# Kernel tuning notes

Hardware: AMD Instinct MI355X
Metric: run time of the kernel (lower is better)

The kernel has to match this reference:

```python
import jax, jax.numpy as jnp
import numpy as np

DT = 1.0 / 120.0
B, T = 2048, 2048


def setup_inputs() -> dict:
    key = jax.random.key(0)
    k1, k2 = jax.random.split(key)
    # friction, damping, restitution (restitution only affects the collision
    # branch, which is not exercised by the non-colliding reference dynamics)
    params = jax.random.uniform(k1, (3,), jnp.float32, 0.05, 0.9)
    # smooth synthetic trajectories: cumulative small steps of [x, y, theta]
    meas = jnp.cumsum(jax.random.normal(k2, (B, T, 3), jnp.float32) * 0.01, axis=1)
    return {"params": params, "measurements": meas}


def _ekf_loss(params, measurements):
    friction, damping = params[0], params[1]
    dt = jnp.asarray(DT, measurements.dtype)
    dtype = measurements.dtype

    R = jnp.diag(jnp.array([2.5e-7, 2.5e-7, 9.1e-3], dtype=dtype))
    Q = jnp.diag(jnp.array([2e-10, 2e-10, 3e-7, 3e-7, 1e-2, 1e-1], dtype=dtype))
    H = jnp.zeros((3, 6), dtype=dtype).at[0, 0].set(1.0).at[1, 1].set(1.0).at[2, 4].set(1.0)
    I6 = jnp.eye(6, dtype=dtype)

    # linearized transition Jacobian (constant-velocity with table damping)
    F = I6
    F = F.at[0, 2].set(dt).at[1, 3].set(dt).at[4, 5].set(dt)
    F = F.at[2, 2].set(1.0 - dt * damping).at[3, 3].set(1.0 - dt * damping)

    def predict_state(s):
        x, y, dx, dy, th, dth = s
        dx2 = dx - dt * (damping * dx + friction * jnp.sign(dx))
        dy2 = dy - dt * (damping * dy + friction * jnp.sign(dy))
        return jnp.stack([x + dx * dt, y + dy * dt, dx2, dy2, th + dth * dt, dth])

    def step(carry, z):
        s, P, acc = carry
        s_pred = predict_state(s)                     # (6,)
        P_pred = F @ P @ F.T + Q                      # (6,6)
        yv = z - H @ s_pred                           # (3,) innovation
        S = H @ P_pred @ H.T + R                      # (3,3)
        Sinv_y = jnp.linalg.solve(S, yv)
        K = jnp.linalg.solve(S.T, (P_pred @ H.T).T).T  # P_pred H^T S^{-1}
        s_new = s_pred + K @ yv
        P_new = (I6 - K @ H) @ P_pred
        # evaluation term: sign*exp(logdet(S)) + y^T S^{-1} y == det(S) + y^T S^{-1} y
        acc = acc + jnp.linalg.det(S) + yv @ Sinv_y
        return (s_new, P_new, acc), None

    def run_one(zs):
        # initial state from finite-difference velocities (as in the source)
        v0 = (zs[1] - zs[0]) / dt
        s0 = jnp.stack([zs[0, 0], zs[0, 1], v0[0], v0[1], zs[0, 2], v0[2]])
        P0 = I6 * 0.01
        (_, _, acc), _ = jax.lax.scan(step, (s0, P0, jnp.zeros((), dtype)), zs[1:])
        return acc / (zs.shape[0] - 1)

    return jnp.mean(jax.vmap(run_one)(measurements))


def reference(params, measurements):
    return _ekf_loss(params, measurements)
```

## Files before the change

kernel.cpp:

```cpp
#include <hip/hip_runtime.h>

#define DTF (1.0f/120.0f)

constexpr int Bn = 2048;
constexpr int Tn = 2048;
constexpr int NS = Tn - 1;
constexpr int ZF = Tn * 3;
constexpr int NCH = 64;
constexpr int LCH = 32;
constexpr int SPAN = 109;
constexpr int NSEG = 14;
constexpr int BT = 64;
constexpr int GX = Bn / BT;
constexpr int NBLK = GX * NCH;
constexpr int LSTR = 66;

__global__ __launch_bounds__(BT, 2) void ekf_main(const float* __restrict__ params,
                                                  const float* __restrict__ meas,
                                                  double* __restrict__ part)
{
    __shared__ float lds[28 * LSTR];

    const int tid = threadIdx.x;
    const int c = blockIdx.y;
    const float dt = DTF;
    const float fric = params[0];
    const float damping = params[1];
    const float a = 1.f - dt * damping;
    const float dfr = dt * fric;
    const float dt2 = dt * dt, a2 = a * a;
    const float qp = 2e-10f, qv = 3e-7f, qth = 1e-2f, qdth = 1e-1f;
    const float Rp = 2.5e-7f, Rt = 9.1e-3f;
    const float* __restrict__ zt = meas + (size_t)(blockIdx.x * BT) * ZF;

    const int j0   = c * LCH;
    const int jend = min(j0 + LCH, NS);
    int jw = jend - SPAN;
    jw = (jw < 3) ? 0 : (jw - ((jw - 3) & 3));
    const int A0 = (jw * 3 + 3) & ~3;
    const int d  = jw * 3 + 3 - A0;
    const int AI = (jw * 3) & ~3;
    const int di = jw * 3 - AI;

    float4 g[7];
#define LOADF(A) do { \
    _Pragma("unroll") \
    for (int i_ = 0; i_ < 7; ++i_) { \
        int flat_ = i_ * BT + tid; \
        int row_ = flat_ / 7, k_ = flat_ - row_ * 7; \
        int fs_ = min((A) + 4 * k_, ZF - 4); \
        g[i_] = *(const float4*)(zt + (size_t)row_ * ZF + fs_); \
    } \
} while (0)
#define STORELDS() do { \
    _Pragma("unroll") \
    for (int i_ = 0; i_ < 7; ++i_) { \
        int flat_ = i_ * BT + tid; \
        int row_ = flat_ / 7, k_ = flat_ - row_ * 7; \
        int base_ = 4 * k_ * LSTR + row_; \
        lds[base_]            = g[i_].x; \
        lds[base_ + LSTR]     = g[i_].y; \
        lds[base_ + 2*LSTR]   = g[i_].z; \
        lds[base_ + 3*LSTR]   = g[i_].w; \
    } \
} while (0)

    LOADF(AI);
    STORELDS();
    float i0 = lds[(di+0)*LSTR + tid], i1 = lds[(di+1)*LSTR + tid], i2 = lds[(di+2)*LSTR + tid];
    float i3 = lds[(di+3)*LSTR + tid], i4 = lds[(di+4)*LSTR + tid], i5 = lds[(di+5)*LSTR + tid];
    float s0 = i0, s1 = i1, s4 = i2;
    float s2 = (i3 - i0) / dt, s3 = (i4 - i1) / dt, s5 = (i5 - i2) / dt;

    float x00 = 0.01f, x01 = 0.f, x11 = 0.01f;
    float t00 = 0.01f, t01 = 0.f, t11 = 0.01f;

    LOADF(A0);
    float facc = 0.f;

    for (int s = 0; s < NSEG; ++s) {
        STORELDS();
        LOADF(A0 + 24 * (s + 1));
        __builtin_amdgcn_sched_barrier(0);
        float zv[24];
        #pragma unroll
        for (int k2 = 0; k2 < 24; ++k2) zv[k2] = lds[(d + k2) * LSTR + tid];
        const int jb = jw + 8 * s;
        #pragma unroll
        for (int ss = 0; ss < 8; ++ss) {
            float Pp00 = fmaf(dt2, x11, fmaf(2.f * dt, x01, x00)) + qp;
            float Pp01 = a * fmaf(dt, x11, x01);
            float Pp11 = fmaf(a2, x11, qv);
            float Sx = Pp00 + Rp;
            float isx = __builtin_amdgcn_rcpf(Sx);
            float kx0 = Pp00 * isx, kx1 = Pp01 * isx;
            x00 = Pp00 - kx0 * Pp00; x01 = Pp01 - kx0 * Pp01; x11 = Pp11 - kx1 * Pp01;
            float Tp00 = fmaf(dt2, t11, fmaf(2.f * dt, t01, t00)) + qth;
            float Tp01 = fmaf(dt, t11, t01);
            float Tp11 = t11 + qdth;
            float St = Tp00 + Rt;
            float ist = __builtin_amdgcn_rcpf(St);
            float kt0 = Tp00 * ist, kt1 = Tp01 * ist;
            t00 = Tp00 - kt0 * Tp00; t01 = Tp01 - kt0 * Tp01; t11 = Tp11 - kt1 * Tp01;
            float det = Sx * Sx * St;
            float p0 = fmaf(dt, s2, s0), p1 = fmaf(dt, s3, s1), p4 = fmaf(dt, s5, s4);
            float p2 = fmaf(a, s2, -copysignf(dfr, s2));
            float p3 = fmaf(a, s3, -copysignf(dfr, s3));
            float y0 = zv[ss*3+0] - p0, y1 = zv[ss*3+1] - p1, y2 = zv[ss*3+2] - p4;
            s0 = fmaf(kx0, y0, p0); s1 = fmaf(kx0, y1, p1);
            s2 = fmaf(kx1, y0, p2); s3 = fmaf(kx1, y1, p3);
            s4 = fmaf(kt0, y2, p4); s5 = fmaf(kt1, y2, s5);
            int j = jb + ss;
            if (j >= j0 && j < jend)
                facc += det + isx * fmaf(y0, y0, y1 * y1) + ist * y2 * y2;
        }
    }
#undef STORELDS
#undef LOADF

    double acc = (double)facc;
    for (int off = 32; off; off >>= 1) acc += __shfl_down(acc, off);
    if (tid == 0) part[blockIdx.y * GX + blockIdx.x] = acc;
}

__global__ void finalize_kernel(const double* __restrict__ part, float* __restrict__ out)
{
    const int tid = threadIdx.x;
    double v = part[tid] + part[tid + 1024];
    for (int off = 32; off; off >>= 1) v += __shfl_down(v, off);
    __shared__ double wp[16];
    if ((tid & 63) == 0) wp[tid >> 6] = v;
    __syncthreads();
    if (tid == 0) {
        double t = 0.0;
        #pragma unroll
        for (int i = 0; i < 16; ++i) t += wp[i];
        out[0] = (float)(t / ((double)Bn * (double)NS));
    }
}

extern "C" void kernel_launch(void* const* d_in, const int* in_sizes, int n_in,
                              void* d_out, int out_size, void* d_ws, size_t ws_size,
                              hipStream_t stream)
{
    const float* params = (const float*)d_in[0];
    const float* meas = (const float*)d_in[1];
    double* part = (double*)d_ws;
    float* out = (float*)d_out;

    hipLaunchKernelGGL(ekf_main, dim3(GX, NCH), dim3(BT), 0, stream, params, meas, part);
    hipLaunchKernelGGL(finalize_kernel, dim3(1), dim3(1024), 0, stream, part, out);
}
```

Before: 39.34 us.

## Precompute shared Kalman gain table once and halve chunk length with more chunks

The covariance and gain recursion does not depend on the measurements, so it is now run once by a single-thread kernel that writes a per-step table of gains, inverse innovations and determinants. The main kernel loads this table into LDS and only does the state update, and chunks shrink to 16 steps over a shorter warm-up span with 128 chunks, plus early exit from segments past the chunk end. This removes the redundant per-thread covariance math and shortens the serial dependency chain per block. In exchange it adds a serial kernel launch on the critical path and relies on the covariance converging within the shorter span, since every chunk reuses the same early-step gains for its warm-up window.

```diff
diff --git a/kernel.cpp b/kernel.cpp
--- a/kernel.cpp
+++ b/kernel.cpp
@@ -6,20 +6,58 @@
 constexpr int Tn = 2048;
 constexpr int NS = Tn - 1;
 constexpr int ZF = Tn * 3;
-constexpr int NCH = 64;
-constexpr int LCH = 32;
-constexpr int SPAN = 109;
-constexpr int NSEG = 14;
+constexpr int NCH = 128;
+constexpr int LCH = 16;
+constexpr int SPAN = 88;
+constexpr int NSEG = 12;
+constexpr int GROWS = NSEG * 8;
 constexpr int BT = 64;
 constexpr int GX = Bn / BT;
 constexpr int NBLK = GX * NCH;
 constexpr int LSTR = 66;
+constexpr int GT_F = GROWS * 8;
 
-__global__ __launch_bounds__(BT, 2) void ekf_main(const float* __restrict__ params,
+constexpr int WS_PART = 4096;
+
+__global__ void gains_kernel(const float* __restrict__ params, float* __restrict__ gt)
+{
+    if (threadIdx.x != 0) return;
+    const float dt = DTF;
+    const float damping = params[1];
+    const float a = 1.f - dt * damping;
+    const float dt2 = dt * dt, a2 = a * a;
+    const float qp = 2e-10f, qv = 3e-7f, qth = 1e-2f, qdth = 1e-1f;
+    const float Rp = 2.5e-7f, Rt = 9.1e-3f;
+    float x00 = 0.01f, x01 = 0.f, x11 = 0.01f;
+    float t00 = 0.01f, t01 = 0.f, t11 = 0.01f;
+    for (int t = 0; t < GROWS; ++t) {
+        float Pp00 = fmaf(dt2, x11, fmaf(2.f * dt, x01, x00)) + qp;
+        float Pp01 = a * fmaf(dt, x11, x01);
+        float Pp11 = fmaf(a2, x11, qv);
+        float Sx = Pp00 + Rp;
+        float isx = __builtin_amdgcn_rcpf(Sx);
+        float kx0 = Pp00 * isx, kx1 = Pp01 * isx;
+        x00 = Pp00 - kx0 * Pp00; x01 = Pp01 - kx0 * Pp01; x11 = Pp11 - kx1 * Pp01;
+        float Tp00 = fmaf(dt2, t11, fmaf(2.f * dt, t01, t00)) + qth;
+        float Tp01 = fmaf(dt, t11, t01);
+        float Tp11 = t11 + qdth;
+        float St = Tp00 + Rt;
+        float ist = __builtin_amdgcn_rcpf(St);
+        float kt0 = Tp00 * ist, kt1 = Tp01 * ist;
+        t00 = Tp00 - kt0 * Tp00; t01 = Tp01 - kt0 * Tp01; t11 = Tp11 - kt1 * Tp01;
+        float* row = gt + (size_t)t * 8;
+        row[0] = kx0; row[1] = kx1; row[2] = kt0; row[3] = kt1;
+        row[4] = isx; row[5] = ist; row[6] = Sx * Sx * St; row[7] = 0.f;
+    }
+}
+
+__global__ __launch_bounds__(BT, 4) void ekf_main(const float* __restrict__ params,
                                                   const float* __restrict__ meas,
+                                                  const float* __restrict__ gt,
                                                   double* __restrict__ part)
 {
     __shared__ float lds[28 * LSTR];
+    __shared__ float gtab[GT_F];
 
     const int tid = threadIdx.x;
     const int c = blockIdx.y;
@@ -28,9 +66,6 @@
     const float damping = params[1];
     const float a = 1.f - dt * damping;
     const float dfr = dt * fric;
-    const float dt2 = dt * dt, a2 = a * a;
-    const float qp = 2e-10f, qv = 3e-7f, qth = 1e-2f, qdth = 1e-1f;
-    const float Rp = 2.5e-7f, Rt = 9.1e-3f;
     const float* __restrict__ zt = meas + (size_t)(blockIdx.x * BT) * ZF;
 
     const int j0   = c * LCH;
@@ -41,6 +76,9 @@
     const int d  = jw * 3 + 3 - A0;
     const int AI = (jw * 3) & ~3;
     const int di = jw * 3 - AI;
+
+    #pragma unroll
+    for (int i = 0; i < GT_F / BT; ++i) gtab[i * BT + tid] = gt[i * BT + tid];
 
     float4 g[7];
 #define LOADF(A) do { \
@@ -72,47 +110,32 @@
     float s0 = i0, s1 = i1, s4 = i2;
     float s2 = (i3 - i0) / dt, s3 = (i4 - i1) / dt, s5 = (i5 - i2) / dt;
 
-    float x00 = 0.01f, x01 = 0.f, x11 = 0.01f;
-    float t00 = 0.01f, t01 = 0.f, t11 = 0.01f;
-
     LOADF(A0);
     float facc = 0.f;
 
     for (int s = 0; s < NSEG; ++s) {
+        const int jb = jw + 8 * s;
+        if (jb >= jend) break;
         STORELDS();
         LOADF(A0 + 24 * (s + 1));
         __builtin_amdgcn_sched_barrier(0);
         float zv[24];
         #pragma unroll
         for (int k2 = 0; k2 < 24; ++k2) zv[k2] = lds[(d + k2) * LSTR + tid];
-        const int jb = jw + 8 * s;
         #pragma unroll
         for (int ss = 0; ss < 8; ++ss) {
-            float Pp00 = fmaf(dt2, x11, fmaf(2.f * dt, x01, x00)) + qp;
-            float Pp01 = a * fmaf(dt, x11, x01);
-            float Pp11 = fmaf(a2, x11, qv);
-            float Sx = Pp00 + Rp;
-            float isx = __builtin_amdgcn_rcpf(Sx);
-            float kx0 = Pp00 * isx, kx1 = Pp01 * isx;
-            x00 = Pp00 - kx0 * Pp00; x01 = Pp01 - kx0 * Pp01; x11 = Pp11 - kx1 * Pp01;
-            float Tp00 = fmaf(dt2, t11, fmaf(2.f * dt, t01, t00)) + qth;
-            float Tp01 = fmaf(dt, t11, t01);
-            float Tp11 = t11 + qdth;
-            float St = Tp00 + Rt;
-            float ist = __builtin_amdgcn_rcpf(St);
-            float kt0 = Tp00 * ist, kt1 = Tp01 * ist;
-            t00 = Tp00 - kt0 * Tp00; t01 = Tp01 - kt0 * Tp01; t11 = Tp11 - kt1 * Tp01;
-            float det = Sx * Sx * St;
+            const float4 ga = *(const float4*)&gtab[(8 * s + ss) * 8];
+            const float4 gb = *(const float4*)&gtab[(8 * s + ss) * 8 + 4];
             float p0 = fmaf(dt, s2, s0), p1 = fmaf(dt, s3, s1), p4 = fmaf(dt, s5, s4);
             float p2 = fmaf(a, s2, -copysignf(dfr, s2));
             float p3 = fmaf(a, s3, -copysignf(dfr, s3));
             float y0 = zv[ss*3+0] - p0, y1 = zv[ss*3+1] - p1, y2 = zv[ss*3+2] - p4;
-            s0 = fmaf(kx0, y0, p0); s1 = fmaf(kx0, y1, p1);
-            s2 = fmaf(kx1, y0, p2); s3 = fmaf(kx1, y1, p3);
-            s4 = fmaf(kt0, y2, p4); s5 = fmaf(kt1, y2, s5);
+            s0 = fmaf(ga.x, y0, p0); s1 = fmaf(ga.x, y1, p1);
+            s2 = fmaf(ga.y, y0, p2); s3 = fmaf(ga.y, y1, p3);
+            s4 = fmaf(ga.z, y2, p4); s5 = fmaf(ga.w, y2, s5);
             int j = jb + ss;
             if (j >= j0 && j < jend)
-                facc += det + isx * fmaf(y0, y0, y1 * y1) + ist * y2 * y2;
+                facc += gb.z + gb.x * fmaf(y0, y0, y1 * y1) + gb.y * y2 * y2;
         }
     }
 #undef STORELDS
@@ -126,7 +149,9 @@
 __global__ void finalize_kernel(const double* __restrict__ part, float* __restrict__ out)
 {
     const int tid = threadIdx.x;
-    double v = part[tid] + part[tid + 1024];
+    double v = 0.0;
+    #pragma unroll
+    for (int i = 0; i < NBLK / 1024; ++i) v += part[tid + i * 1024];
     for (int off = 32; off; off >>= 1) v += __shfl_down(v, off);
     __shared__ double wp[16];
     if ((tid & 63) == 0) wp[tid >> 6] = v;
@@ -145,9 +170,11 @@
 {
     const float* params = (const float*)d_in[0];
     const float* meas = (const float*)d_in[1];
-    double* part = (double*)d_ws;
+    float* gt = (float*)d_ws;
+    double* part = (double*)((char*)d_ws + WS_PART);
     float* out = (float*)d_out;
 
-    hipLaunchKernelGGL(ekf_main, dim3(GX, NCH), dim3(BT), 0, stream, params, meas, part);
+    hipLaunchKernelGGL(gains_kernel, dim3(1), dim3(64), 0, stream, params, gt);
+    hipLaunchKernelGGL(ekf_main, dim3(GX, NCH), dim3(BT), 0, stream, params, meas, gt, part);
     hipLaunchKernelGGL(finalize_kernel, dim3(1), dim3(1024), 0, stream, part, out);
 }
```

Result: slower. 58.27 us (+48.1%).

## Use steady-state Kalman gains for non-head chunks and row-major LDS layout

Applied to the files above, without the earlier changes.

Since the covariance recursion is data-independent and converges, non-head chunks run 48 covariance iterations up front and then use constant gains, determinant and inverse innovation variances. The per-step covariance and reciprocal work drops out of the main loop, and the quadratic terms are summed separately and scaled once at the end. The LDS layout becomes row-major with float2 accesses, the loop exits early once the chunk's rows are done, and launch bounds rise to 4 blocks per CU. This relies on the covariance having converged within the warmup window, so it is approximate near the converged limit.

```diff
diff --git a/kernel.cpp b/kernel.cpp
--- a/kernel.cpp
+++ b/kernel.cpp
@@ -8,18 +8,18 @@
 constexpr int ZF = Tn * 3;
 constexpr int NCH = 64;
 constexpr int LCH = 32;
-constexpr int SPAN = 109;
+constexpr int SPAN = 108;
 constexpr int NSEG = 14;
 constexpr int BT = 64;
 constexpr int GX = Bn / BT;
 constexpr int NBLK = GX * NCH;
-constexpr int LSTR = 66;
-
-__global__ __launch_bounds__(BT, 2) void ekf_main(const float* __restrict__ params,
+constexpr int RSTR = 30;
+
+__global__ __launch_bounds__(BT, 4) void ekf_main(const float* __restrict__ params,
                                                   const float* __restrict__ meas,
                                                   double* __restrict__ part)
 {
-    __shared__ float lds[28 * LSTR];
+    __shared__ float lds[BT * RSTR];
 
     const int tid = threadIdx.x;
     const int c = blockIdx.y;
@@ -33,90 +33,137 @@
     const float Rp = 2.5e-7f, Rt = 9.1e-3f;
     const float* __restrict__ zt = meas + (size_t)(blockIdx.x * BT) * ZF;
 
-    const int j0   = c * LCH;
+    const int j0 = c * LCH;
     const int jend = min(j0 + LCH, NS);
     int jw = jend - SPAN;
     jw = (jw < 3) ? 0 : (jw - ((jw - 3) & 3));
     const int A0 = (jw * 3 + 3) & ~3;
-    const int d  = jw * 3 + 3 - A0;
-    const int AI = (jw * 3) & ~3;
-    const int di = jw * 3 - AI;
+    const int r0 = j0 - jw, r1 = jend - jw;
+    const bool head = (jw == 0);
+
+    int row_[7], k4_[7];
+    #pragma unroll
+    for (int i = 0; i < 7; ++i) {
+        int flat = i * BT + tid;
+        int row = flat / 7;
+        row_[i] = row; k4_[i] = 4 * (flat - row * 7);
+    }
 
     float4 g[7];
 #define LOADF(A) do { \
     _Pragma("unroll") \
     for (int i_ = 0; i_ < 7; ++i_) { \
-        int flat_ = i_ * BT + tid; \
-        int row_ = flat_ / 7, k_ = flat_ - row_ * 7; \
-        int fs_ = min((A) + 4 * k_, ZF - 4); \
-        g[i_] = *(const float4*)(zt + (size_t)row_ * ZF + fs_); \
-    } \
-} while (0)
+        int fs_ = min((A) + k4_[i_], ZF - 4); \
+        g[i_] = *(const float4*)(zt + (size_t)row_[i_] * ZF + fs_); \
+    } } while (0)
 #define STORELDS() do { \
     _Pragma("unroll") \
     for (int i_ = 0; i_ < 7; ++i_) { \
-        int flat_ = i_ * BT + tid; \
-        int row_ = flat_ / 7, k_ = flat_ - row_ * 7; \
-        int base_ = 4 * k_ * LSTR + row_; \
-        lds[base_]            = g[i_].x; \
-        lds[base_ + LSTR]     = g[i_].y; \
-        lds[base_ + 2*LSTR]   = g[i_].z; \
-        lds[base_ + 3*LSTR]   = g[i_].w; \
-    } \
-} while (0)
-
-    LOADF(AI);
-    STORELDS();
-    float i0 = lds[(di+0)*LSTR + tid], i1 = lds[(di+1)*LSTR + tid], i2 = lds[(di+2)*LSTR + tid];
-    float i3 = lds[(di+3)*LSTR + tid], i4 = lds[(di+4)*LSTR + tid], i5 = lds[(di+5)*LSTR + tid];
-    float s0 = i0, s1 = i1, s4 = i2;
-    float s2 = (i3 - i0) / dt, s3 = (i4 - i1) / dt, s5 = (i5 - i2) / dt;
-
-    float x00 = 0.01f, x01 = 0.f, x11 = 0.01f;
-    float t00 = 0.01f, t01 = 0.f, t11 = 0.01f;
+        float* p_ = &lds[row_[i_] * RSTR + k4_[i_]]; \
+        *(float2*)p_       = make_float2(g[i_].x, g[i_].y); \
+        *(float2*)(p_ + 2) = make_float2(g[i_].z, g[i_].w); \
+    } } while (0)
 
     LOADF(A0);
-    float facc = 0.f;
-
-    for (int s = 0; s < NSEG; ++s) {
-        STORELDS();
-        LOADF(A0 + 24 * (s + 1));
-        __builtin_amdgcn_sched_barrier(0);
-        float zv[24];
-        #pragma unroll
-        for (int k2 = 0; k2 < 24; ++k2) zv[k2] = lds[(d + k2) * LSTR + tid];
-        const int jb = jw + 8 * s;
-        #pragma unroll
-        for (int ss = 0; ss < 8; ++ss) {
-            float Pp00 = fmaf(dt2, x11, fmaf(2.f * dt, x01, x00)) + qp;
+
+    float ckx0, ckx1, ckt0, ckt1, cisx, cist, cdet;
+    {
+        float x00=0.01f, x01=0.f, x11=0.01f, t00=0.01f, t01=0.f, t11=0.01f;
+        for (int t = 0; t < 48; ++t) {
+            float Pp00 = fmaf(dt2, x11, fmaf(2.f*dt, x01, x00)) + qp;
             float Pp01 = a * fmaf(dt, x11, x01);
             float Pp11 = fmaf(a2, x11, qv);
-            float Sx = Pp00 + Rp;
-            float isx = __builtin_amdgcn_rcpf(Sx);
-            float kx0 = Pp00 * isx, kx1 = Pp01 * isx;
-            x00 = Pp00 - kx0 * Pp00; x01 = Pp01 - kx0 * Pp01; x11 = Pp11 - kx1 * Pp01;
-            float Tp00 = fmaf(dt2, t11, fmaf(2.f * dt, t01, t00)) + qth;
+            float Sx = Pp00 + Rp, isx = __builtin_amdgcn_rcpf(Sx);
+            float kx0 = Pp00*isx, kx1 = Pp01*isx;
+            x00 = Pp00-kx0*Pp00; x01 = Pp01-kx0*Pp01; x11 = Pp11-kx1*Pp01;
+            float Tp00 = fmaf(dt2, t11, fmaf(2.f*dt, t01, t00)) + qth;
             float Tp01 = fmaf(dt, t11, t01);
             float Tp11 = t11 + qdth;
-            float St = Tp00 + Rt;
-            float ist = __builtin_amdgcn_rcpf(St);
-            float kt0 = Tp00 * ist, kt1 = Tp01 * ist;
-            t00 = Tp00 - kt0 * Tp00; t01 = Tp01 - kt0 * Tp01; t11 = Tp11 - kt1 * Tp01;
-            float det = Sx * Sx * St;
-            float p0 = fmaf(dt, s2, s0), p1 = fmaf(dt, s3, s1), p4 = fmaf(dt, s5, s4);
-            float p2 = fmaf(a, s2, -copysignf(dfr, s2));
-            float p3 = fmaf(a, s3, -copysignf(dfr, s3));
-            float y0 = zv[ss*3+0] - p0, y1 = zv[ss*3+1] - p1, y2 = zv[ss*3+2] - p4;
-            s0 = fmaf(kx0, y0, p0); s1 = fmaf(kx0, y1, p1);
-            s2 = fmaf(kx1, y0, p2); s3 = fmaf(kx1, y1, p3);
-            s4 = fmaf(kt0, y2, p4); s5 = fmaf(kt1, y2, s5);
-            int j = jb + ss;
-            if (j >= j0 && j < jend)
-                facc += det + isx * fmaf(y0, y0, y1 * y1) + ist * y2 * y2;
+            float St = Tp00 + Rt, ist = __builtin_amdgcn_rcpf(St);
+            float kt0 = Tp00*ist, kt1 = Tp01*ist;
+            t00 = Tp00-kt0*Tp00; t01 = Tp01-kt0*Tp01; t11 = Tp11-kt1*Tp01;
+            ckx0=kx0; ckx1=kx1; ckt0=kt0; ckt1=kt1; cisx=isx; cist=ist; cdet=Sx*Sx*St;
         }
     }
+
+    STORELDS();
+    float b0 = lds[tid*RSTR+0], b1 = lds[tid*RSTR+1], b2 = lds[tid*RSTR+2];
+    float b3 = lds[tid*RSTR+3], b4 = lds[tid*RSTR+4], b5 = lds[tid*RSTR+5];
+    float s0 = b0, s1 = b1, s4 = b2;
+    float s2 = (b3-b0)/dt, s3 = (b4-b1)/dt, s5 = (b5-b2)/dt;
+
+    LOADF(A0 + 24);
+
+    float facc = 0.f;
+    float accP = 0.f, accT = 0.f, accD = 0.f;
+    float hx00=0.01f, hx01=0.f, hx11=0.01f, ht00=0.01f, ht01=0.f, ht11=0.01f;
+
+#define PREDICT(ZV, SS) \
+    float p0 = fmaf(dt, s2, s0), p1 = fmaf(dt, s3, s1), p4 = fmaf(dt, s5, s4); \
+    float p2 = fmaf(a, s2, -copysignf(dfr, s2)); \
+    float p3 = fmaf(a, s3, -copysignf(dfr, s3)); \
+    float y0 = ZV[3*(SS)] - p0, y1 = ZV[3*(SS)+1] - p1, y2 = ZV[3*(SS)+2] - p4;
+
+#define UPDATE(KX0,KX1,KT0,KT1) \
+    s0 = fmaf(KX0, y0, p0); s1 = fmaf(KX0, y1, p1); \
+    s2 = fmaf(KX1, y0, p2); s3 = fmaf(KX1, y1, p3); \
+    s4 = fmaf(KT0, y2, p4); s5 = fmaf(KT1, y2, s5);
+
+    for (int s = 0; ; ++s) {
+        __builtin_amdgcn_sched_barrier(0);
+        if (!head) {
+            float zv[24];
+            #pragma unroll
+            for (int m = 0; m < 12; ++m) {
+                float2 q = *(const float2*)&lds[tid*RSTR + 2*m];
+                zv[2*m] = q.x; zv[2*m+1] = q.y;
+            }
+            #pragma unroll
+            for (int ss = 0; ss < 8; ++ss) {
+                PREDICT(zv, ss)
+                UPDATE(ckx0, ckx1, ckt0, ckt1)
+                int r = 8*s + ss;
+                if (r >= r0 && r < r1) {
+                    accP = fmaf(y0, y0, fmaf(y1, y1, accP));
+                    accT = fmaf(y2, y2, accT);
+                    accD += cdet;
+                }
+            }
+        } else {
+            float zv[24];
+            #pragma unroll
+            for (int k2 = 0; k2 < 24; ++k2) zv[k2] = lds[tid*RSTR + 3 + k2];
+            #pragma unroll
+            for (int ss = 0; ss < 8; ++ss) {
+                float Pp00 = fmaf(dt2, hx11, fmaf(2.f*dt, hx01, hx00)) + qp;
+                float Pp01 = a * fmaf(dt, hx11, hx01);
+                float Pp11 = fmaf(a2, hx11, qv);
+                float Sx = Pp00 + Rp, isx = __builtin_amdgcn_rcpf(Sx);
+                float kx0 = Pp00*isx, kx1 = Pp01*isx;
+                hx00 = Pp00-kx0*Pp00; hx01 = Pp01-kx0*Pp01; hx11 = Pp11-kx1*Pp01;
+                float Tp00 = fmaf(dt2, ht11, fmaf(2.f*dt, ht01, ht00)) + qth;
+                float Tp01 = fmaf(dt, ht11, ht01);
+                float Tp11 = ht11 + qdth;
+                float St = Tp00 + Rt, ist = __builtin_amdgcn_rcpf(St);
+                float kt0 = Tp00*ist, kt1 = Tp01*ist;
+                ht00 = Tp00-kt0*Tp00; ht01 = Tp01-kt0*Tp01; ht11 = Tp11-kt1*Tp01;
+                PREDICT(zv, ss)
+                UPDATE(kx0, kx1, kt0, kt1)
+                int r = 8*s + ss;
+                if (r >= r0 && r < r1)
+                    facc += Sx*Sx*St + isx*fmaf(y0, y0, y1*y1) + ist*y2*y2;
+            }
+        }
+        if (8*(s+1) >= r1 || s+1 >= NSEG) break;
+        STORELDS();
+        LOADF(A0 + 24*(s+2));
+    }
+#undef UPDATE
+#undef PREDICT
 #undef STORELDS
 #undef LOADF
+
+    if (!head) facc = accD + cisx*accP + cist*accT;
 
     double acc = (double)facc;
     for (int off = 32; off; off >>= 1) acc += __shfl_down(acc, off);
```

New measurement: 52.82 us. +34.3%, slower.

## Use converged steady-state Kalman gains for non-head chunks with 64-step warmup

Applied to the files above, without the earlier changes.

Splits time into 64-step chunks per wave, four waves per block. Non-head chunks skip the covariance recursion and instead use constant gains, innovation weights and determinant, obtained by iterating the covariance 48 steps up front. The state is warmed up over the previous chunk. Loads are coalesced into double-buffered LDS tiles. This removes most per-step covariance arithmetic and redundant overlap work, but relies on the covariance converging, so accuracy depends on the input dynamics.

```diff
diff --git a/kernel.cpp b/kernel.cpp
--- a/kernel.cpp
+++ b/kernel.cpp
@@ -2,139 +2,169 @@
 
 #define DTF (1.0f/120.0f)
 
-constexpr int Bn = 2048;
-constexpr int Tn = 2048;
-constexpr int NS = Tn - 1;
-constexpr int ZF = Tn * 3;
-constexpr int NCH = 64;
-constexpr int LCH = 32;
-constexpr int SPAN = 109;
-constexpr int NSEG = 14;
-constexpr int BT = 64;
-constexpr int GX = Bn / BT;
-constexpr int NBLK = GX * NCH;
-constexpr int LSTR = 66;
+constexpr int Bn = 2048, Tn = 2048, NS = Tn - 1, ZF = Tn * 3;
+constexpr int BT = 256;
+constexpr int NCG = 8;
+constexpr int NBG = Bn / 64;
+constexpr int NBLK = NBG * NCG;
+constexpr int TSTR = 97;
+constexpr int SEGF = 64 * TSTR;
 
-__global__ __launch_bounds__(BT, 2) void ekf_main(const float* __restrict__ params,
+__global__ __launch_bounds__(BT, 1) void ekf_main(const float* __restrict__ params,
                                                   const float* __restrict__ meas,
                                                   double* __restrict__ part)
 {
-    __shared__ float lds[28 * LSTR];
+    __shared__ float tile[2 * SEGF];
+    __shared__ double wsum[4];
 
-    const int tid = threadIdx.x;
-    const int c = blockIdx.y;
-    const float dt = DTF;
-    const float fric = params[0];
-    const float damping = params[1];
-    const float a = 1.f - dt * damping;
-    const float dfr = dt * fric;
+    const int tid = threadIdx.x, w = tid >> 6, lane = tid & 63;
+    const int bg = blockIdx.x & 31, cg = blockIdx.x >> 5;
+    const int c = 4 * cg + w;
+    const float dt = DTF, fric = params[0], damping = params[1];
+    const float a = 1.f - dt * damping, dfr = dt * fric;
     const float dt2 = dt * dt, a2 = a * a;
     const float qp = 2e-10f, qv = 3e-7f, qth = 1e-2f, qdth = 1e-1f;
     const float Rp = 2.5e-7f, Rt = 9.1e-3f;
-    const float* __restrict__ zt = meas + (size_t)(blockIdx.x * BT) * ZF;
+    const float* __restrict__ zb = meas + (size_t)bg * 64 * ZF;
 
-    const int j0   = c * LCH;
-    const int jend = min(j0 + LCH, NS);
-    int jw = jend - SPAN;
-    jw = (jw < 3) ? 0 : (jw - ((jw - 3) & 3));
-    const int A0 = (jw * 3 + 3) & ~3;
-    const int d  = jw * 3 + 3 - A0;
-    const int AI = (jw * 3) & ~3;
-    const int di = jw * 3 - AI;
+    const int Z0 = (cg == 0) ? 0 : 64 * (4 * cg - 1);
+    const int nseg = (cg == 0) ? 9 : 11;
+    const int jw = 64 * max(c - 1, 0);
+    const int j0own = 64 * c;
+    const int jend = min(64 * c + 64, NS);
+    const bool head = (c <= 1);
 
-    float4 g[7];
-#define LOADF(A) do { \
+#define LOADSEG(Rx, S) do { \
+    int zs_ = Z0 + 32 * (S); \
     _Pragma("unroll") \
-    for (int i_ = 0; i_ < 7; ++i_) { \
-        int flat_ = i_ * BT + tid; \
-        int row_ = flat_ / 7, k_ = flat_ - row_ * 7; \
-        int fs_ = min((A) + 4 * k_, ZF - 4); \
-        g[i_] = *(const float4*)(zt + (size_t)row_ * ZF + fs_); \
-    } \
-} while (0)
-#define STORELDS() do { \
+    for (int k_ = 0; k_ < 24; ++k_) { \
+        int f_ = tid + 256 * k_; \
+        int r_ = f_ / 96, col_ = f_ - 96 * r_; \
+        int gi_ = min(3 * zs_ + col_, ZF - 1); \
+        Rx[k_] = zb[(size_t)r_ * ZF + gi_]; \
+    } } while (0)
+
+#define WRITESEG(Rx, BUF) do { \
+    float* tb_ = &tile[(BUF) * SEGF]; \
     _Pragma("unroll") \
-    for (int i_ = 0; i_ < 7; ++i_) { \
-        int flat_ = i_ * BT + tid; \
-        int row_ = flat_ / 7, k_ = flat_ - row_ * 7; \
-        int base_ = 4 * k_ * LSTR + row_; \
-        lds[base_]            = g[i_].x; \
-        lds[base_ + LSTR]     = g[i_].y; \
-        lds[base_ + 2*LSTR]   = g[i_].z; \
-        lds[base_ + 3*LSTR]   = g[i_].w; \
-    } \
-} while (0)
+    for (int k_ = 0; k_ < 24; ++k_) { \
+        int f_ = tid + 256 * k_; \
+        int r_ = f_ / 96, col_ = f_ - 96 * r_; \
+        tb_[r_ * TSTR + col_] = Rx[k_]; \
+    } } while (0)
 
-    LOADF(AI);
-    STORELDS();
-    float i0 = lds[(di+0)*LSTR + tid], i1 = lds[(di+1)*LSTR + tid], i2 = lds[(di+2)*LSTR + tid];
-    float i3 = lds[(di+3)*LSTR + tid], i4 = lds[(di+4)*LSTR + tid], i5 = lds[(di+5)*LSTR + tid];
-    float s0 = i0, s1 = i1, s4 = i2;
-    float s2 = (i3 - i0) / dt, s3 = (i4 - i1) / dt, s5 = (i5 - i2) / dt;
+    float R0[24], R1[24];
+    LOADSEG(R0, 0);
+    LOADSEG(R1, 1);
 
-    float x00 = 0.01f, x01 = 0.f, x11 = 0.01f;
-    float t00 = 0.01f, t01 = 0.f, t11 = 0.01f;
-
-    LOADF(A0);
-    float facc = 0.f;
-
-    for (int s = 0; s < NSEG; ++s) {
-        STORELDS();
-        LOADF(A0 + 24 * (s + 1));
-        __builtin_amdgcn_sched_barrier(0);
-        float zv[24];
-        #pragma unroll
-        for (int k2 = 0; k2 < 24; ++k2) zv[k2] = lds[(d + k2) * LSTR + tid];
-        const int jb = jw + 8 * s;
-        #pragma unroll
-        for (int ss = 0; ss < 8; ++ss) {
+    float ckx0, ckx1, ckt0, ckt1, cisx, cist, cdet;
+    {
+        float x00 = 0.01f, x01 = 0.f, x11 = 0.01f, t00 = 0.01f, t01 = 0.f, t11 = 0.01f;
+        for (int t = 0; t < 48; ++t) {
             float Pp00 = fmaf(dt2, x11, fmaf(2.f * dt, x01, x00)) + qp;
             float Pp01 = a * fmaf(dt, x11, x01);
             float Pp11 = fmaf(a2, x11, qv);
-            float Sx = Pp00 + Rp;
-            float isx = __builtin_amdgcn_rcpf(Sx);
+            float Sx = Pp00 + Rp, isx = __builtin_amdgcn_rcpf(Sx);
             float kx0 = Pp00 * isx, kx1 = Pp01 * isx;
             x00 = Pp00 - kx0 * Pp00; x01 = Pp01 - kx0 * Pp01; x11 = Pp11 - kx1 * Pp01;
             float Tp00 = fmaf(dt2, t11, fmaf(2.f * dt, t01, t00)) + qth;
             float Tp01 = fmaf(dt, t11, t01);
             float Tp11 = t11 + qdth;
-            float St = Tp00 + Rt;
-            float ist = __builtin_amdgcn_rcpf(St);
+            float St = Tp00 + Rt, ist = __builtin_amdgcn_rcpf(St);
             float kt0 = Tp00 * ist, kt1 = Tp01 * ist;
             t00 = Tp00 - kt0 * Tp00; t01 = Tp01 - kt0 * Tp01; t11 = Tp11 - kt1 * Tp01;
-            float det = Sx * Sx * St;
-            float p0 = fmaf(dt, s2, s0), p1 = fmaf(dt, s3, s1), p4 = fmaf(dt, s5, s4);
-            float p2 = fmaf(a, s2, -copysignf(dfr, s2));
-            float p3 = fmaf(a, s3, -copysignf(dfr, s3));
-            float y0 = zv[ss*3+0] - p0, y1 = zv[ss*3+1] - p1, y2 = zv[ss*3+2] - p4;
-            s0 = fmaf(kx0, y0, p0); s1 = fmaf(kx0, y1, p1);
-            s2 = fmaf(kx1, y0, p2); s3 = fmaf(kx1, y1, p3);
-            s4 = fmaf(kt0, y2, p4); s5 = fmaf(kt1, y2, s5);
-            int j = jb + ss;
-            if (j >= j0 && j < jend)
-                facc += det + isx * fmaf(y0, y0, y1 * y1) + ist * y2 * y2;
+            ckx0 = kx0; ckx1 = kx1; ckt0 = kt0; ckt1 = kt1;
+            cisx = isx; cist = ist; cdet = Sx * Sx * St;
         }
     }
-#undef STORELDS
-#undef LOADF
+
+    WRITESEG(R0, 0);
+    __syncthreads();
+
+    float s0 = 0.f, s1 = 0.f, s2 = 0.f, s3 = 0.f, s4 = 0.f, s5 = 0.f;
+    float hx00 = 0.01f, hx01 = 0.f, hx11 = 0.01f;
+    float ht00 = 0.01f, ht01 = 0.f, ht11 = 0.01f;
+    float facc = 0.f;
+
+    for (int s = 0; s < nseg; ++s) {
+        if (s + 1 < nseg) { if (((s + 1) & 1) == 1) WRITESEG(R1, 1); else WRITESEG(R0, 0); }
+        if (s + 2 < nseg) { if ((s & 1) == 0) LOADSEG(R0, s + 2); else LOADSEG(R1, s + 2); }
+
+        const int zs = Z0 + 32 * s;
+        const float* tb = &tile[(s & 1) * SEGF + lane * TSTR];
+        if (jw >= zs && jw < zs + 32) {
+            int d0 = 3 * (jw - zs);
+            float z0 = tb[d0], z1 = tb[d0+1], z2 = tb[d0+2];
+            float z3 = tb[d0+3], z4 = tb[d0+4], z5 = tb[d0+5];
+            s0 = z0; s1 = z1; s4 = z2;
+            s2 = (z3 - z0) / dt; s3 = (z4 - z1) / dt; s5 = (z5 - z2) / dt;
+        }
+        const int jA = max(jw, zs - 1), jB = min(jend, zs + 31);
+        if (head) {
+            #pragma unroll 4
+            for (int j = jA; j < jB; ++j) {
+                int d = 3 * (j + 1 - zs);
+                float z0 = tb[d], z1 = tb[d+1], z2 = tb[d+2];
+                float Pp00 = fmaf(dt2, hx11, fmaf(2.f*dt, hx01, hx00)) + qp;
+                float Pp01 = a * fmaf(dt, hx11, hx01);
+                float Pp11 = fmaf(a2, hx11, qv);
+                float Sx = Pp00 + Rp, isx = __builtin_amdgcn_rcpf(Sx);
+                float kx0 = Pp00 * isx, kx1 = Pp01 * isx;
+                hx00 = Pp00 - kx0*Pp00; hx01 = Pp01 - kx0*Pp01; hx11 = Pp11 - kx1*Pp01;
+                float Tp00 = fmaf(dt2, ht11, fmaf(2.f*dt, ht01, ht00)) + qth;
+                float Tp01 = fmaf(dt, ht11, ht01);
+                float Tp11 = ht11 + qdth;
+                float St = Tp00 + Rt, ist = __builtin_amdgcn_rcpf(St);
+                float kt0 = Tp00 * ist, kt1 = Tp01 * ist;
+                ht00 = Tp00 - kt0*Tp00; ht01 = Tp01 - kt0*Tp01; ht11 = Tp11 - kt1*Tp01;
+                float p0 = fmaf(dt, s2, s0), p1 = fmaf(dt, s3, s1), p4 = fmaf(dt, s5, s4);
+                float p2 = fmaf(a, s2, -copysignf(dfr, s2));
+                float p3 = fmaf(a, s3, -copysignf(dfr, s3));
+                float y0 = z0 - p0, y1 = z1 - p1, y2 = z2 - p4;
+                s0 = fmaf(kx0, y0, p0); s1 = fmaf(kx0, y1, p1);
+                s2 = fmaf(kx1, y0, p2); s3 = fmaf(kx1, y1, p3);
+                s4 = fmaf(kt0, y2, p4); s5 = fmaf(kt1, y2, s5);
+                if (j >= j0own)
+                    facc += Sx*Sx*St + isx * fmaf(y0, y0, y1*y1) + ist * y2*y2;
+            }
+        } else {
+            #pragma unroll 4
+            for (int j = jA; j < jB; ++j) {
+                int d = 3 * (j + 1 - zs);
+                float z0 = tb[d], z1 = tb[d+1], z2 = tb[d+2];
+                float p0 = fmaf(dt, s2, s0), p1 = fmaf(dt, s3, s1), p4 = fmaf(dt, s5, s4);
+                float p2 = fmaf(a, s2, -copysignf(dfr, s2));
+                float p3 = fmaf(a, s3, -copysignf(dfr, s3));
+                float y0 = z0 - p0, y1 = z1 - p1, y2 = z2 - p4;
+                s0 = fmaf(ckx0, y0, p0); s1 = fmaf(ckx0, y1, p1);
+                s2 = fmaf(ckx1, y0, p2); s3 = fmaf(ckx1, y1, p3);
+                s4 = fmaf(ckt0, y2, p4); s5 = fmaf(ckt1, y2, s5);
+                if (j >= j0own)
+                    facc += cdet + cisx * fmaf(y0, y0, y1*y1) + cist * y2*y2;
+            }
+        }
+        __syncthreads();
+    }
+#undef WRITESEG
+#undef LOADSEG
 
     double acc = (double)facc;
     for (int off = 32; off; off >>= 1) acc += __shfl_down(acc, off);
-    if (tid == 0) part[blockIdx.y * GX + blockIdx.x] = acc;
+    if (lane == 0) wsum[w] = acc;
+    __syncthreads();
+    if (tid == 0) part[blockIdx.x] = wsum[0] + wsum[1] + wsum[2] + wsum[3];
 }
 
 __global__ void finalize_kernel(const double* __restrict__ part, float* __restrict__ out)
 {
     const int tid = threadIdx.x;
-    double v = part[tid] + part[tid + 1024];
+    double v = part[tid];
     for (int off = 32; off; off >>= 1) v += __shfl_down(v, off);
-    __shared__ double wp[16];
+    __shared__ double wp[4];
     if ((tid & 63) == 0) wp[tid >> 6] = v;
     __syncthreads();
     if (tid == 0) {
-        double t = 0.0;
-        #pragma unroll
-        for (int i = 0; i < 16; ++i) t += wp[i];
+        double t = wp[0] + wp[1] + wp[2] + wp[3];
         out[0] = (float)(t / ((double)Bn * (double)NS));
     }
 }
@@ -148,6 +178,6 @@
     double* part = (double*)d_ws;
     float* out = (float*)d_out;
 
-    hipLaunchKernelGGL(ekf_main, dim3(GX, NCH), dim3(BT), 0, stream, params, meas, part);
-    hipLaunchKernelGGL(finalize_kernel, dim3(1), dim3(1024), 0, stream, part, out);
+    hipLaunchKernelGGL(ekf_main, dim3(NBLK), dim3(BT), 0, stream, params, meas, part);
+    hipLaunchKernelGGL(finalize_kernel, dim3(1), dim3(256), 0, stream, part, out);
 }
```

Result: slower. 43.87 us (+11.5%).
